# Kernel tuning notes

Measured on AMD Instinct MI355X. Metric: run time of the kernel, lower is better.

## Reference

```python
import jax, jax.numpy as jnp
import numpy as np

MODES1 = 16
WIDTH = 64
EMB_DIM = 1024
PADDING = 2


def setup_inputs() -> dict:
    key = jax.random.key(0)
    ks = jax.random.split(key, 7)
    B, L = 64, 8192
    token = jax.random.normal(ks[0], (B, EMB_DIM), dtype=jnp.float32)
    # decode_head: Linear(emb_dim -> width*modes1*2)
    w_dec = jax.random.normal(ks[1], (EMB_DIM, WIDTH * MODES1 * 2), dtype=jnp.float32) / np.sqrt(EMB_DIM)
    b_dec = jax.random.normal(ks[2], (WIDTH * MODES1 * 2,), dtype=jnp.float32) * 0.01
    # fc1: Linear(width -> 128), fc2: Linear(128 -> 1)
    w1 = jax.random.normal(ks[3], (WIDTH, 128), dtype=jnp.float32) / np.sqrt(WIDTH)
    b1 = jax.random.normal(ks[4], (128,), dtype=jnp.float32) * 0.01
    w2 = jax.random.normal(ks[5], (128, 1), dtype=jnp.float32) / np.sqrt(128)
    b2 = jax.random.normal(ks[6], (1,), dtype=jnp.float32) * 0.01
    return {"token": token, "x_len": L, "w_dec": w_dec, "b_dec": b_dec,
            "w1": w1, "b1": b1, "w2": w2, "b2": b2}


def reference(token, x_len, w_dec, b_dec, w1, b1, w2, b2):
    B = token.shape[0]
    # decode_head projection -> [B, width, modes1, 2] -> complex modes
    h = token @ w_dec + b_dec
    h = h.reshape(B, WIDTH, MODES1, 2)
    modes = jax.lax.complex(h[..., 0], h[..., 1])  # [B, width, modes1]
    # zero-pad spectrum to L//2+1 bins, inverse rFFT to length L
    n_freq = x_len // 2 + 1
    out_ft = jnp.zeros((B, WIDTH, n_freq), dtype=jnp.complex64)
    out_ft = out_ft.at[:, :, :MODES1].set(modes)
    x = jnp.fft.irfft(out_ft, n=x_len, axis=-1)  # [B, width, L]
    # drop padding, move channels last
    x = x[..., :-PADDING].transpose(0, 2, 1)  # [B, L-2, width]
    # MLP head
    x = jax.nn.gelu(x @ w1 + b1, approximate=False)
    x = x @ w2 + b2  # [B, L-2, 1]
    # torch .squeeze(-2): only squeezes if that dim is 1
    if x.shape[-2] == 1:
        x = jnp.squeeze(x, axis=-2)
    return x
```

## Files before the change

kernel.cpp:

```cpp
#include <hip/hip_runtime.h>
#include <cstdint>

#define B_    64
#define EMB   1024
#define NO    2048
#define NL    8192
#define LOUT  8190
#define NJ    128
#define NKC   16
#define KCH   64
#define ALPHA 0.3989422804014327f

__global__ __launch_bounds__(256) void k1_gemm(const float* __restrict__ token,
                                               const float* __restrict__ wdec,
                                               float* __restrict__ c_part) {
    const int ot  = blockIdx.x & 31;
    const int kc  = blockIdx.x >> 5;
    const int o0  = ot * 64;
    const int kb  = kc * KCH;
    const int tid = threadIdx.x;
    const int og  = tid & 15;
    const int bg  = tid >> 4;

    __shared__ float tokT[KCH][68];
    __shared__ float wdS[KCH][68];

    {
        const int k4 = tid & 15;
        const int b0 = tid >> 4;
#pragma unroll
        for (int i = 0; i < 4; ++i) {
            int b = b0 + i * 16;
            float4 v = *(const float4*)&token[b * EMB + kb + k4 * 4];
            tokT[k4 * 4 + 0][b] = v.x;
            tokT[k4 * 4 + 1][b] = v.y;
            tokT[k4 * 4 + 2][b] = v.z;
            tokT[k4 * 4 + 3][b] = v.w;
        }
        const int o4 = tid & 15;
        const int k0 = tid >> 4;
#pragma unroll
        for (int i = 0; i < 4; ++i) {
            int k = k0 + i * 16;
            *(float4*)&wdS[k][o4 * 4] = *(const float4*)&wdec[(kb + k) * NO + o0 + o4 * 4];
        }
    }
    __syncthreads();

    float acc[4][4] = {};
#pragma unroll 4
    for (int k = 0; k < KCH; ++k) {
        float4 tv = *(const float4*)&tokT[k][bg * 4];
        float4 wv = *(const float4*)&wdS[k][og * 4];
        acc[0][0] = fmaf(tv.x, wv.x, acc[0][0]);
        acc[0][1] = fmaf(tv.x, wv.y, acc[0][1]);
        acc[0][2] = fmaf(tv.x, wv.z, acc[0][2]);
        acc[0][3] = fmaf(tv.x, wv.w, acc[0][3]);
        acc[1][0] = fmaf(tv.y, wv.x, acc[1][0]);
        acc[1][1] = fmaf(tv.y, wv.y, acc[1][1]);
        acc[1][2] = fmaf(tv.y, wv.z, acc[1][2]);
        acc[1][3] = fmaf(tv.y, wv.w, acc[1][3]);
        acc[2][0] = fmaf(tv.z, wv.x, acc[2][0]);
        acc[2][1] = fmaf(tv.z, wv.y, acc[2][1]);
        acc[2][2] = fmaf(tv.z, wv.z, acc[2][2]);
        acc[2][3] = fmaf(tv.z, wv.w, acc[2][3]);
        acc[3][0] = fmaf(tv.w, wv.x, acc[3][0]);
        acc[3][1] = fmaf(tv.w, wv.y, acc[3][1]);
        acc[3][2] = fmaf(tv.w, wv.z, acc[3][2]);
        acc[3][3] = fmaf(tv.w, wv.w, acc[3][3]);
    }

    float* cp = c_part + kc * (B_ * NO) + o0 + og * 4;
#pragma unroll
    for (int ib = 0; ib < 4; ++ib) {
        float4 v = {acc[ib][0], acc[ib][1], acc[ib][2], acc[ib][3]};
        *(float4*)&cp[(bg * 4 + ib) * NO] = v;
    }
}

__global__ __launch_bounds__(256) void k2_fused(const float* __restrict__ c_part,
                                                const float* __restrict__ bdec,
                                                const float* __restrict__ w1,
                                                const float* __restrict__ b1,
                                                const float* __restrict__ w2,
                                                const float* __restrict__ b2,
                                                float* __restrict__ F_part) {
    const int b  = blockIdx.x >> 2;
    const int q4 = blockIdx.x & 3;
    const int j0 = q4 * 32;
    const int t  = threadIdx.x;

    __shared__ float cwS[2048];
    __shared__ float w1S[2048];
    __shared__ float w2S[32], b1S[32];
    __shared__ float aspec[32 * 32];
    __shared__ float FpS[4][64];

    {
        const float4* cp4 = (const float4*)c_part;
        const float4* bd4 = (const float4*)bdec;
#pragma unroll
        for (int i = 0; i < 2; ++i) {
            int s = t + i * 256;
            float4 v = bd4[s];
#pragma unroll
            for (int kc = 0; kc < NKC; ++kc) {
                float4 c = cp4[kc * 32768 + b * 512 + s];
                v.x += c.x; v.y += c.y; v.z += c.z; v.w += c.w;
            }
            ((float4*)cwS)[s] = v;
        }
#pragma unroll
        for (int i = 0; i < 8; ++i) {
            int e = t + i * 256;
            int w = e >> 5, jl = e & 31;
            w1S[e] = w1[w * 128 + j0 + jl];
        }
        if (t < 32) { w2S[t] = w2[j0 + t]; b1S[t] = b1[j0 + t]; }
    }
    __syncthreads();

    {
        const int m4 = t & 7, jl = t >> 3;
        float4 acc = {0.f, 0.f, 0.f, 0.f};
        const float4* cw4 = (const float4*)cwS;
        for (int w = 0; w < 64; ++w) {
            float4 cv = cw4[w * 8 + m4];
            float  wv = w1S[w * 32 + jl];
            acc.x = fmaf(cv.x, wv, acc.x);
            acc.y = fmaf(cv.y, wv, acc.y);
            acc.z = fmaf(cv.z, wv, acc.z);
            acc.w = fmaf(cv.w, wv, acc.w);
        }
        const float s2 = 2.0f / NL;
        if (m4 == 0) {
            acc.x = acc.x * (1.0f / NL) + b1S[jl];
            acc.y = 0.f;
            acc.z *= s2; acc.w *= -s2;
        } else {
            acc.x *= s2; acc.y *= -s2; acc.z *= s2; acc.w *= -s2;
        }
        ((float4*)aspec)[jl * 8 + m4] = acc;
    }
    __syncthreads();

    {
        const int m  = t & 31;
        const int jq = t >> 5;
        float rc = 0.f, rs = 0.f;
        for (int r = 0; r < 4; ++r) {
            const int jl = r * 8 + jq;
            const float* A = aspec + jl * 32;
            const float C0 = A[0];
            float Qc, Qs, lc, ls;
            if (m == 0) {
                float ssum = 0.f;
#pragma unroll
                for (int k = 1; k <= 15; ++k)
                    ssum += A[2 * k] * A[2 * k] + A[2 * k + 1] * A[2 * k + 1];
                Qc = fmaf(C0, C0, 0.5f * ssum);
                Qs = 0.f; lc = C0; ls = 0.f;
            } else {
                lc = (m <= 15) ? A[2 * m]     : 0.f;
                ls = (m <= 15) ? A[2 * m + 1] : 0.f;
                Qc = 2.f * C0 * lc;
                Qs = 2.f * C0 * ls;
                int lo = m - 15; if (lo < 1)  lo = 1;
                int hi = m - 1;  if (hi > 15) hi = 15;
                for (int k1 = lo; k1 <= hi; ++k1) {
                    int k2 = m - k1;
                    float c1 = A[2 * k1], s1 = A[2 * k1 + 1];
                    float c2 = A[2 * k2], sv = A[2 * k2 + 1];
                    Qc = fmaf(0.5f, fmaf(c1, c2, -s1 * sv), Qc);
                    Qs = fmaf(0.5f, fmaf(c1, sv,  s1 * c2), Qs);
                }
                for (int k = 1; k <= 15 - m; ++k) {
                    float ch = A[2 * (k + m)], sh = A[2 * (k + m) + 1];
                    float cl = A[2 * k],       sl = A[2 * k + 1];
                    Qc = fmaf(ch, cl, Qc); Qc = fmaf(sh, sl, Qc);
                    Qs = fmaf(sh, cl, Qs); Qs = fmaf(-ch, sl, Qs);
                }
            }
            const float wj = w2S[jl];
            rc += wj * fmaf(ALPHA, Qc, 0.5f * lc);
            rs += wj * fmaf(ALPHA, Qs, 0.5f * ls);
        }
        rc += __shfl_xor(rc, 32);
        rs += __shfl_xor(rs, 32);
        if ((t & 32) == 0) {
            FpS[t >> 6][m]      = rc;
            FpS[t >> 6][32 + m] = rs;
        }
    }
    __syncthreads();
    if (t < 32) {
        float Fc = FpS[0][t] + FpS[1][t] + FpS[2][t] + FpS[3][t];
        float Fs = FpS[0][32 + t] + FpS[1][32 + t] + FpS[2][32 + t] + FpS[3][32 + t];
        if (t == 0 && q4 == 0) Fc += b2[0];
        F_part[blockIdx.x * 64 + t]      = Fc;
        F_part[blockIdx.x * 64 + 32 + t] = Fs;
    }
}

__global__ __launch_bounds__(256) void k3_eval(const float* __restrict__ F_part,
                                               float* __restrict__ out) {
    const int b     = blockIdx.x >> 4;
    const int chunk = blockIdx.x & 15;
    __shared__ float Fsh[64];
    if (threadIdx.x < 64) {
        const float* Fb = F_part + b * 256 + threadIdx.x;
        Fsh[threadIdx.x] = Fb[0] + Fb[64] + Fb[128] + Fb[192];
    }
    __syncthreads();

    const float w0 = 6.283185307179586f / (float)NL;
#pragma unroll
    for (int i = 0; i < 2; ++i) {
        int t = chunk * 512 + i * 256 + threadIdx.x;
        if (t < LOUT) {
            float s1, c1;
            __sincosf(w0 * (float)t, &s1, &c1);
            float acc = Fsh[0];
            acc = fmaf(Fsh[1], c1, acc);
            acc = fmaf(Fsh[33], s1, acc);
            float ckm = 1.f, ck = c1, skm = 0.f, sk = s1;
            float tc = 2.f * c1;
#pragma unroll
            for (int k = 2; k <= 30; ++k) {
                float cn = fmaf(tc, ck, -ckm);
                float sn = fmaf(tc, sk, -skm);
                acc = fmaf(Fsh[k], cn, acc);
                acc = fmaf(Fsh[32 + k], sn, acc);
                ckm = ck; ck = cn;
                skm = sk; sk = sn;
            }
            out[b * LOUT + t] = acc;
        }
    }
}

extern "C" void kernel_launch(void* const* d_in, const int* in_sizes, int n_in,
                              void* d_out, int out_size, void* d_ws, size_t ws_size,
                              hipStream_t stream) {
    const float* token = (const float*)d_in[0];
    const float* wdec  = (const float*)d_in[2];
    const float* bdec  = (const float*)d_in[3];
    const float* w1    = (const float*)d_in[4];
    const float* b1    = (const float*)d_in[5];
    const float* w2    = (const float*)d_in[6];
    const float* b2    = (const float*)d_in[7];
    float* out = (float*)d_out;

    float* c_part = (float*)d_ws;
    float* F_part = c_part + NKC * B_ * NO;

    k1_gemm<<<512, 256, 0, stream>>>(token, wdec, c_part);
    k2_fused<<<256, 256, 0, stream>>>(c_part, bdec, w1, b1, w2, b2, F_part);
    k3_eval<<<1024, 256, 0, stream>>>(F_part, out);
}
```

Baseline: 100.4 us.

## Exploit quarter-period symmetry in trig eval and merge k2 hidden-unit blocks

```diff
diff --git a/kernel.cpp b/kernel.cpp
--- a/kernel.cpp
+++ b/kernel.cpp
@@ -78,79 +78,82 @@
     }
 }
 
-__global__ __launch_bounds__(256) void k2_fused(const float* __restrict__ c_part,
+__global__ __launch_bounds__(512) void k2_fused(const float* __restrict__ c_part,
                                                 const float* __restrict__ bdec,
                                                 const float* __restrict__ w1,
                                                 const float* __restrict__ b1,
                                                 const float* __restrict__ w2,
                                                 const float* __restrict__ b2,
-                                                float* __restrict__ F_part) {
-    const int b  = blockIdx.x >> 2;
-    const int q4 = blockIdx.x & 3;
-    const int j0 = q4 * 32;
-    const int t  = threadIdx.x;
+                                                float* __restrict__ F) {
+    const int b = blockIdx.x;
+    const int t = threadIdx.x;
 
     __shared__ float cwS[2048];
-    __shared__ float w1S[2048];
-    __shared__ float w2S[32], b1S[32];
-    __shared__ float aspec[32 * 32];
-    __shared__ float FpS[4][64];
+    __shared__ float w1S[8192];
+    __shared__ float b1S[128], w2S[128];
+    __shared__ float aspec[128 * 32];
+    __shared__ float FpS[8][64];
 
     {
         const float4* cp4 = (const float4*)c_part;
         const float4* bd4 = (const float4*)bdec;
-#pragma unroll
-        for (int i = 0; i < 2; ++i) {
-            int s = t + i * 256;
-            float4 v = bd4[s];
-#pragma unroll
-            for (int kc = 0; kc < NKC; ++kc) {
-                float4 c = cp4[kc * 32768 + b * 512 + s];
-                v.x += c.x; v.y += c.y; v.z += c.z; v.w += c.w;
-            }
-            ((float4*)cwS)[s] = v;
-        }
-#pragma unroll
-        for (int i = 0; i < 8; ++i) {
-            int e = t + i * 256;
-            int w = e >> 5, jl = e & 31;
-            w1S[e] = w1[w * 128 + j0 + jl];
-        }
-        if (t < 32) { w2S[t] = w2[j0 + t]; b1S[t] = b1[j0 + t]; }
-    }
-    __syncthreads();
-
-    {
-        const int m4 = t & 7, jl = t >> 3;
-        float4 acc = {0.f, 0.f, 0.f, 0.f};
+        float4 v = bd4[t];
+#pragma unroll
+        for (int kc = 0; kc < NKC; ++kc) {
+            float4 c = cp4[kc * 32768 + b * 512 + t];
+            v.x += c.x; v.y += c.y; v.z += c.z; v.w += c.w;
+        }
+        ((float4*)cwS)[t] = v;
+        const float4* w14 = (const float4*)w1;
+#pragma unroll
+        for (int i = 0; i < 4; ++i)
+            ((float4*)w1S)[t + i * 512] = w14[t + i * 512];
+        if (t < 128) { b1S[t] = b1[t]; w2S[t] = w2[t]; }
+    }
+    __syncthreads();
+
+    {
+        const int m4 = t & 7, j1 = t >> 3;
+        float4 a0 = {0.f, 0.f, 0.f, 0.f};
+        float4 a1 = {0.f, 0.f, 0.f, 0.f};
         const float4* cw4 = (const float4*)cwS;
         for (int w = 0; w < 64; ++w) {
             float4 cv = cw4[w * 8 + m4];
-            float  wv = w1S[w * 32 + jl];
-            acc.x = fmaf(cv.x, wv, acc.x);
-            acc.y = fmaf(cv.y, wv, acc.y);
-            acc.z = fmaf(cv.z, wv, acc.z);
-            acc.w = fmaf(cv.w, wv, acc.w);
+            float  w0v = w1S[w * 128 + j1];
+            float  w1v = w1S[w * 128 + j1 + 64];
+            a0.x = fmaf(cv.x, w0v, a0.x);
+            a0.y = fmaf(cv.y, w0v, a0.y);
+            a0.z = fmaf(cv.z, w0v, a0.z);
+            a0.w = fmaf(cv.w, w0v, a0.w);
+            a1.x = fmaf(cv.x, w1v, a1.x);
+            a1.y = fmaf(cv.y, w1v, a1.y);
+            a1.z = fmaf(cv.z, w1v, a1.z);
+            a1.w = fmaf(cv.w, w1v, a1.w);
         }
         const float s2 = 2.0f / NL;
         if (m4 == 0) {
-            acc.x = acc.x * (1.0f / NL) + b1S[jl];
-            acc.y = 0.f;
-            acc.z *= s2; acc.w *= -s2;
+            a0.x = a0.x * (1.0f / NL) + b1S[j1];
+            a0.y = 0.f;
+            a0.z *= s2; a0.w *= -s2;
+            a1.x = a1.x * (1.0f / NL) + b1S[j1 + 64];
+            a1.y = 0.f;
+            a1.z *= s2; a1.w *= -s2;
         } else {
-            acc.x *= s2; acc.y *= -s2; acc.z *= s2; acc.w *= -s2;
-        }
-        ((float4*)aspec)[jl * 8 + m4] = acc;
+            a0.x *= s2; a0.y *= -s2; a0.z *= s2; a0.w *= -s2;
+            a1.x *= s2; a1.y *= -s2; a1.z *= s2; a1.w *= -s2;
+        }
+        ((float4*)aspec)[j1 * 8 + m4]        = a0;
+        ((float4*)aspec)[(j1 + 64) * 8 + m4] = a1;
     }
     __syncthreads();
 
     {
         const int m  = t & 31;
-        const int jq = t >> 5;
+        const int jg = t >> 5;
         float rc = 0.f, rs = 0.f;
-        for (int r = 0; r < 4; ++r) {
-            const int jl = r * 8 + jq;
-            const float* A = aspec + jl * 32;
+        for (int r = 0; r < 8; ++r) {
+            const int j = r * 16 + jg;
+            const float* A = aspec + j * 32;
             const float C0 = A[0];
             float Qc, Qs, lc, ls;
             if (m == 0) {
@@ -181,7 +184,7 @@
                     Qs = fmaf(sh, cl, Qs); Qs = fmaf(-ch, sl, Qs);
                 }
             }
-            const float wj = w2S[jl];
+            const float wj = w2S[j];
             rc += wj * fmaf(ALPHA, Qc, 0.5f * lc);
             rs += wj * fmaf(ALPHA, Qs, 0.5f * ls);
         }
@@ -193,49 +196,58 @@
         }
     }
     __syncthreads();
-    if (t < 32) {
-        float Fc = FpS[0][t] + FpS[1][t] + FpS[2][t] + FpS[3][t];
-        float Fs = FpS[0][32 + t] + FpS[1][32 + t] + FpS[2][32 + t] + FpS[3][32 + t];
-        if (t == 0 && q4 == 0) Fc += b2[0];
-        F_part[blockIdx.x * 64 + t]      = Fc;
-        F_part[blockIdx.x * 64 + 32 + t] = Fs;
-    }
-}
-
-__global__ __launch_bounds__(256) void k3_eval(const float* __restrict__ F_part,
+    if (t < 64) {
+        float Fv = 0.f;
+#pragma unroll
+        for (int w = 0; w < 8; ++w) Fv += FpS[w][t];
+        if (t == 0) Fv += b2[0];
+        F[b * 64 + t] = Fv;
+    }
+}
+
+__global__ __launch_bounds__(256) void k3_eval(const float* __restrict__ F,
                                                float* __restrict__ out) {
-    const int b     = blockIdx.x >> 4;
-    const int chunk = blockIdx.x & 15;
+    const int b     = blockIdx.x >> 2;
+    const int chunk = blockIdx.x & 3;
     __shared__ float Fsh[64];
-    if (threadIdx.x < 64) {
-        const float* Fb = F_part + b * 256 + threadIdx.x;
-        Fsh[threadIdx.x] = Fb[0] + Fb[64] + Fb[128] + Fb[192];
-    }
+    if (threadIdx.x < 64) Fsh[threadIdx.x] = F[b * 64 + threadIdx.x];
     __syncthreads();
 
     const float w0 = 6.283185307179586f / (float)NL;
 #pragma unroll
     for (int i = 0; i < 2; ++i) {
         int t = chunk * 512 + i * 256 + threadIdx.x;
-        if (t < LOUT) {
-            float s1, c1;
-            __sincosf(w0 * (float)t, &s1, &c1);
-            float acc = Fsh[0];
-            acc = fmaf(Fsh[1], c1, acc);
-            acc = fmaf(Fsh[33], s1, acc);
-            float ckm = 1.f, ck = c1, skm = 0.f, sk = s1;
-            float tc = 2.f * c1;
-#pragma unroll
-            for (int k = 2; k <= 30; ++k) {
-                float cn = fmaf(tc, ck, -ckm);
-                float sn = fmaf(tc, sk, -skm);
-                acc = fmaf(Fsh[k], cn, acc);
-                acc = fmaf(Fsh[32 + k], sn, acc);
-                ckm = ck; ck = cn;
-                skm = sk; sk = sn;
+        float s1, c1;
+        __sincosf(w0 * (float)t, &s1, &c1);
+        float A0 = 0.f, A1 = 0.f, A2 = 0.f, A3 = 0.f, B1 = 0.f, B3 = 0.f;
+        float ckm = 1.f, ck = c1, skm = 0.f, sk = s1;
+        const float tc = 2.f * c1;
+#pragma unroll
+        for (int k = 1; k <= 30; ++k) {
+            const float fc = Fsh[k], fs = Fsh[32 + k];
+            if ((k & 3) == 0) {
+                A0 = fmaf(fc, ck, A0); A0 = fmaf(fs, sk, A0);
+            } else if ((k & 3) == 1) {
+                A1 = fmaf(fc, ck, A1); A1 = fmaf(fs, sk, A1);
+                B1 = fmaf(fs, ck, B1); B1 = fmaf(-fc, sk, B1);
+            } else if ((k & 3) == 2) {
+                A2 = fmaf(fc, ck, A2); A2 = fmaf(fs, sk, A2);
+            } else {
+                A3 = fmaf(fc, ck, A3); A3 = fmaf(fs, sk, A3);
+                B3 = fmaf(fs, ck, B3); B3 = fmaf(-fc, sk, B3);
             }
-            out[b * LOUT + t] = acc;
-        }
+            float cn = fmaf(tc, ck, -ckm);
+            float sn = fmaf(tc, sk, -skm);
+            ckm = ck; ck = cn;
+            skm = sk; sk = sn;
+        }
+        const float S = Fsh[0] + A0;
+        float* ob = out + b * LOUT;
+        ob[t]        = S + A1 + A2 + A3;
+        ob[t + 2048] = S + B1 - A2 - B3;
+        ob[t + 4096] = S - A1 + A2 - A3;
+        if (t < LOUT - 6144)
+            ob[t + 6144] = S - B1 - A2 + B3;
     }
 }
 
@@ -252,9 +264,9 @@
     float* out = (float*)d_out;
 
     float* c_part = (float*)d_ws;
-    float* F_part = c_part + NKC * B_ * NO;
+    float* F      = c_part + NKC * B_ * NO;
 
     k1_gemm<<<512, 256, 0, stream>>>(token, wdec, c_part);
-    k2_fused<<<256, 256, 0, stream>>>(c_part, bdec, w1, b1, w2, b2, F_part);
-    k3_eval<<<1024, 256, 0, stream>>>(F_part, out);
-}
+    k2_fused<<<64, 512, 0, stream>>>(c_part, bdec, w1, b1, w2, b2, F);
+    k3_eval<<<256, 256, 0, stream>>>(F, out);
+}
```

Result: slower. 141.3 us (+40.7%).
